# Optimization experiments

Hardware: AMD Instinct MI355X
Metric: run time of the kernel (lower is better)

## Reference

```python
import jax, jax.numpy as jnp
import numpy as np

HC = 64                 # half_context
PAD = HC + 3            # padding_idx row of positional table
NEG = 1.0e12            # additive mask constant from the torch code


def setup_inputs() -> dict:
    key = jax.random.key(0)
    ks = jax.random.split(key, 7)
    B, S, D, C = 32, 2048, 1024, 256
    embeds = jax.random.normal(ks[0], (B, S, D), dtype=jnp.float32)
    embeds_mask = jnp.ones((B, S), dtype=jnp.float32)
    latent = jax.random.normal(ks[1], (C, D), dtype=jnp.float32)
    att_diag = jax.random.normal(ks[2], (D,), dtype=jnp.float32)
    tok_diag = jax.random.normal(ks[3], (D,), dtype=jnp.float32)
    pos_table = jax.random.normal(ks[4], (2 * HC + 4, D), dtype=jnp.float32)
    pos_table = pos_table.at[PAD].set(0.0)  # padding_idx row is zeros
    tok_mult = jnp.ones((1,), dtype=jnp.float32)
    rel_pos_ids = jax.random.randint(ks[5], (B, S), 0, HC + 4, dtype=jnp.int32)
    return {
        "embeds": embeds,
        "embeds_mask": embeds_mask,
        "latent": latent,
        "att_diag": att_diag,
        "tok_diag": tok_diag,
        "pos_table": pos_table,
        "tok_mult": tok_mult,
        "rel_pos_ids": rel_pos_ids,
    }


def reference(embeds, embeds_mask, latent, att_diag, tok_diag, pos_table, tok_mult, rel_pos_ids):
    # positional-embedding gather and merge (dropouts are identity in eval)
    absolute_pos = rel_pos_ids + HC                       # [B,S]
    pos_embeds = pos_table[absolute_pos]                  # [B,S,D]
    merged = tok_mult[0] * embeds + pos_embeds            # [B,S,D]
    # entity-token attention scores: (latent * diag) @ merged^T
    scores = jnp.einsum('cd,bsd->bcs', latent * att_diag, merged)  # [B,C,S]
    m = embeds_mask[:, None, :]                           # [B,1,S]
    scores = scores * m + (m - 1.0) * NEG                 # mask-add
    top = jnp.max(scores, axis=1)                         # max over classes -> [B,S]
    att_probs = jax.nn.softmax(top, axis=1)               # softmax over tokens
    # weighted sum of (embeds * tok_diag) by attention probs -> [B,D]
    ctx_vecs = jnp.einsum('bsd,d,bs->bd', embeds, tok_diag, att_probs)
    return ctx_vecs
```

## Files before the change

### kernel.cpp

```cpp
#include <hip/hip_runtime.h>
#include <hip/hip_bf16.h>


#define HC 64
#define NEGV 1000000000000.0f

constexpr int Bb = 32, Ss = 2048, Dd = 1024, Cc = 256;
constexpr int NKC = 32;
constexpr int CT = Cc / 16;
constexpr int NBLK = 16;

typedef _Float16 f16x8 __attribute__((ext_vector_type(8)));
typedef float    f32x4 __attribute__((ext_vector_type(4)));

__global__ __launch_bounds__(256) void k_prep_w(
    const float* __restrict__ latent, const float* __restrict__ att_diag,
    _Float16* __restrict__ whi)
{
    const int idx = blockIdx.x * 256 + threadIdx.x;
    const int c = idx >> 10, k = idx & 1023;
    const float wv = latent[idx] * att_diag[k];
    const int kc = k >> 5, g = (k >> 3) & 3, i = k & 7;
    const int lane = (c & 15) + 16 * g, ct = c >> 4;
    whi[(size_t)kc * 8192 + (size_t)ct * 512 + lane * 8 + i] = (_Float16)wv;
}

__global__ __launch_bounds__(256, 2) void k_scores_mfma(
    const float* __restrict__ embeds,
    const float* __restrict__ mask,
    const float* __restrict__ pos_table,
    const float* __restrict__ tok_mult,
    const int*   __restrict__ rel_ids,
    const _Float16* __restrict__ whi,
    float* __restrict__ partial,
    float* __restrict__ mblk,
    float* __restrict__ zblk)
{
    __shared__ _Float16 sbuf[2][8192];
    __shared__ float l_sh[128];
    __shared__ float w_sh[128];
    __shared__ float red2[2];
    __shared__ float zred[2];

    const int t  = threadIdx.x;
    const int wv = t >> 6;
    const int l  = t & 63;
    const int lr = l & 15;
    const int lg = l >> 4;

    const int b   = blockIdx.x >> 4;
    const int blk = blockIdx.x & 15;
    const int s0  = blk * 128;

    const float tm = tok_mult[0];

    const float* erow[2];
    const float* prow[2];
    #pragma unroll
    for (int st = 0; st < 2; st++) {
        const int tok = s0 + wv * 32 + st * 16 + lr;
        erow[st] = embeds + ((size_t)b * Ss + tok) * Dd;
        prow[st] = pos_table + (size_t)(rel_ids[b * Ss + tok] + HC) * Dd;
    }

    f32x4 acc[CT][2];
    #pragma unroll
    for (int ct = 0; ct < CT; ct++)
        #pragma unroll
        for (int st = 0; st < 2; st++) acc[ct][st] = (f32x4){0.f, 0.f, 0.f, 0.f};

    f32x4 e0[2], e1[2], p0[2], p1[2];
    auto loadEP = [&](int kc) {
        const int k0 = kc * 32 + lg * 8;
        #pragma unroll
        for (int st = 0; st < 2; st++) {
            e0[st] = *(const f32x4*)(erow[st] + k0);
            e1[st] = *(const f32x4*)(erow[st] + k0 + 4);
            p0[st] = *(const f32x4*)(prow[st] + k0);
            p1[st] = *(const f32x4*)(prow[st] + k0 + 4);
        }
    };

    auto stage = [&](int kc, _Float16* dst) {
        const _Float16* src = whi + (size_t)kc * 8192;
        #pragma unroll
        for (int i = 0; i < 4; i++) {
            const int off = (i * 4 + wv) << 9;
            __builtin_amdgcn_global_load_lds(
                (const __attribute__((address_space(1))) void*)(src + off + l * 8),
                (__attribute__((address_space(3))) void*)(dst + off),
                16, 0, 0);
        }
    };

    stage(0, sbuf[0]);
    loadEP(0);
    asm volatile("s_waitcnt vmcnt(8)" ::: "memory");
    __builtin_amdgcn_s_barrier();

    int cur = 0;
    for (int kc = 0; kc < NKC; kc++) {
        if (kc + 1 < NKC) stage(kc + 1, sbuf[cur ^ 1]);

        f16x8 bh[2], bl[2];
        #pragma unroll
        for (int st = 0; st < 2; st++) {
            float e[8], p[8];
            *(f32x4*)&e[0] = e0[st]; *(f32x4*)&e[4] = e1[st];
            *(f32x4*)&p[0] = p0[st]; *(f32x4*)&p[4] = p1[st];
            #pragma unroll
            for (int i = 0; i < 8; i++) {
                const float x = fmaf(tm, e[i], p[i]);
                const _Float16 h = (_Float16)x;
                bh[st][i] = h;
                bl[st][i] = (_Float16)(x - (float)h);
            }
        }
        if (kc + 1 < NKC) loadEP(kc + 1);

        const _Float16* base = sbuf[cur];
        #pragma unroll
        for (int ct = 0; ct < CT; ct++) {
            const f16x8 ah = *(const f16x8*)(base + ct * 512 + l * 8);
            #pragma unroll
            for (int st = 0; st < 2; st++) {
                acc[ct][st] = __builtin_amdgcn_mfma_f32_16x16x32_f16(ah, bh[st], acc[ct][st], 0, 0, 0);
                acc[ct][st] = __builtin_amdgcn_mfma_f32_16x16x32_f16(ah, bl[st], acc[ct][st], 0, 0, 0);
            }
        }
        asm volatile("s_waitcnt vmcnt(8)" ::: "memory");
        __builtin_amdgcn_s_barrier();
        cur ^= 1;
    }

    #pragma unroll
    for (int st = 0; st < 2; st++) {
        float mx = acc[0][st][0];
        #pragma unroll
        for (int ct = 0; ct < CT; ct++)
            #pragma unroll
            for (int r = 0; r < 4; r++) mx = fmaxf(mx, acc[ct][st][r]);
        mx = fmaxf(mx, __shfl_xor(mx, 16));
        mx = fmaxf(mx, __shfl_xor(mx, 32));
        if (lg == 0) {
            const int si = wv * 32 + st * 16 + lr;
            const int s  = s0 + si;
            const float mk = mask[b * Ss + s];
            l_sh[si] = mx * mk + (mk - 1.0f) * NEGV;
        }
    }
    __syncthreads();

    if (t < 128) {
        float v = l_sh[t];
        #pragma unroll
        for (int o = 32; o >= 1; o >>= 1) v = fmaxf(v, __shfl_xor(v, o));
        if ((t & 63) == 0) red2[t >> 6] = v;
    }
    __syncthreads();
    const float Mb = fmaxf(red2[0], red2[1]);
    if (t < 128) w_sh[t] = expf(l_sh[t] - Mb);
    __syncthreads();
    if (t < 128) {
        float z = w_sh[t];
        #pragma unroll
        for (int o = 32; o >= 1; o >>= 1) z += __shfl_xor(z, o);
        if ((t & 63) == 0) zred[t >> 6] = z;
    }
    __syncthreads();

    {
        const float* eb = embeds + ((size_t)b * Ss + s0) * Dd + t * 4;
        f32x4 ca = (f32x4){0.f, 0.f, 0.f, 0.f};
        #pragma unroll 8
        for (int s = 0; s < 128; s++) {
            const float wgt = w_sh[s];
            const f32x4 ev = *(const f32x4*)(eb + (size_t)s * Dd);
            ca[0] = fmaf(wgt, ev[0], ca[0]);
            ca[1] = fmaf(wgt, ev[1], ca[1]);
            ca[2] = fmaf(wgt, ev[2], ca[2]);
            ca[3] = fmaf(wgt, ev[3], ca[3]);
        }
        *(f32x4*)(partial + ((size_t)(b * NBLK + blk)) * Dd + t * 4) = ca;
        if (t == 0) {
            mblk[b * NBLK + blk] = Mb;
            zblk[b * NBLK + blk] = zred[0] + zred[1];
        }
    }
}

__global__ __launch_bounds__(256) void k_finish(
    const float* __restrict__ mblk, const float* __restrict__ zblk,
    const float* __restrict__ partial, const float* __restrict__ tok_diag,
    float* __restrict__ out)
{
    __shared__ float cf[NBLK];
    const int b = blockIdx.x, t = threadIdx.x;

    if (t < 64) {
        const float mv = (t < NBLK) ? mblk[b * NBLK + t] : -3.4e38f;
        float M = mv;
        #pragma unroll
        for (int o = 32; o >= 1; o >>= 1) M = fmaxf(M, __shfl_xor(M, o));
        const float zv = (t < NBLK) ? zblk[b * NBLK + t] * expf(mv - M) : 0.f;
        float Z = zv;
        #pragma unroll
        for (int o = 32; o >= 1; o >>= 1) Z += __shfl_xor(Z, o);
        if (t < NBLK) cf[t] = expf(mv - M) / Z;
    }
    __syncthreads();

    const int d = t * 4;
    f32x4 a = (f32x4){0.f, 0.f, 0.f, 0.f};
    #pragma unroll
    for (int j = 0; j < NBLK; j++) {
        const float c = cf[j];
        const f32x4 p = *(const f32x4*)(partial + ((size_t)(b * NBLK + j)) * Dd + d);
        a[0] = fmaf(c, p[0], a[0]);
        a[1] = fmaf(c, p[1], a[1]);
        a[2] = fmaf(c, p[2], a[2]);
        a[3] = fmaf(c, p[3], a[3]);
    }
    const f32x4 td = *(const f32x4*)(tok_diag + d);
    f32x4 o = a * td;
    *(f32x4*)(out + (size_t)b * Dd + d) = o;
}

extern "C" void kernel_launch(void* const* d_in, const int* in_sizes, int n_in,
                              void* d_out, int out_size, void* d_ws, size_t ws_size,
                              hipStream_t stream) {
    const float* embeds    = (const float*)d_in[0];
    const float* mask      = (const float*)d_in[1];
    const float* latent    = (const float*)d_in[2];
    const float* att_diag  = (const float*)d_in[3];
    const float* tok_diag  = (const float*)d_in[4];
    const float* pos_table = (const float*)d_in[5];
    const float* tok_mult  = (const float*)d_in[6];
    const int*   rel_ids   = (const int*)d_in[7];
    float* out = (float*)d_out;

    char* ws = (char*)d_ws;
    _Float16* whi    = (_Float16*)(ws);
    float*    partial= (float*)(ws + 524288);
    float*    mblk   = (float*)(ws + 2621440);
    float*    zblk   = (float*)(ws + 2623488);

    k_prep_w<<<(Cc * Dd) / 256, 256, 0, stream>>>(latent, att_diag, whi);
    k_scores_mfma<<<Bb * NBLK, 256, 0, stream>>>(
        embeds, mask, pos_table, tok_mult, rel_ids, whi, partial, mblk, zblk);
    k_finish<<<Bb, 256, 0, stream>>>(mblk, zblk, partial, tok_diag, out);
}
```

Measured before the change: 121.9 us.

## Split class tiles across two waves per token group with 512-thread blocks

Doubles the block to 512 threads and splits the 256 classes between wave pairs, so each wave holds half the accumulators (8 tiles instead of 16). Per-wave register use drops, which allows launch bounds of 4 blocks per CU and more waves to hide memory latency. Positional rows are now loaded inside the loop instead of prefetched, and each token sub-tile is converted and multiplied in turn. The cost is that embeds and positional rows are loaded twice, once per class half, and an extra shared-memory max merge is needed.

After: 194.6 us. +59.6%, slower.

```diff
diff --git a/kernel.cpp b/kernel.cpp
--- a/kernel.cpp
+++ b/kernel.cpp
@@ -7,11 +7,11 @@
 
 constexpr int Bb = 32, Ss = 2048, Dd = 1024, Cc = 256;
 constexpr int NKC = 32;
-constexpr int CT = Cc / 16;
 constexpr int NBLK = 16;
 
 typedef _Float16 f16x8 __attribute__((ext_vector_type(8)));
 typedef float    f32x4 __attribute__((ext_vector_type(4)));
+typedef float    f32x2 __attribute__((ext_vector_type(2)));
 
 __global__ __launch_bounds__(256) void k_prep_w(
     const float* __restrict__ latent, const float* __restrict__ att_diag,
@@ -25,7 +25,7 @@
     whi[(size_t)kc * 8192 + (size_t)ct * 512 + lane * 8 + i] = (_Float16)wv;
 }
 
-__global__ __launch_bounds__(256, 2) void k_scores_mfma(
+__global__ __launch_bounds__(512, 4) void k_scores_mfma(
     const float* __restrict__ embeds,
     const float* __restrict__ mask,
     const float* __restrict__ pos_table,
@@ -37,13 +37,14 @@
     float* __restrict__ zblk)
 {
     __shared__ _Float16 sbuf[2][8192];
-    __shared__ float l_sh[128];
+    __shared__ float red[2][128];
     __shared__ float w_sh[128];
-    __shared__ float red2[2];
-    __shared__ float zred[2];
+    __shared__ float red2[2], zred[2];
 
     const int t  = threadIdx.x;
-    const int wv = t >> 6;
+    const int wvid = t >> 6;
+    const int cg = wvid & 1;
+    const int tg = wvid >> 1;
     const int l  = t & 63;
     const int lr = l & 15;
     const int lg = l >> 4;
@@ -58,34 +59,32 @@
     const float* prow[2];
     #pragma unroll
     for (int st = 0; st < 2; st++) {
-        const int tok = s0 + wv * 32 + st * 16 + lr;
+        const int tok = s0 + tg * 32 + st * 16 + lr;
         erow[st] = embeds + ((size_t)b * Ss + tok) * Dd;
         prow[st] = pos_table + (size_t)(rel_ids[b * Ss + tok] + HC) * Dd;
     }
 
-    f32x4 acc[CT][2];
-    #pragma unroll
-    for (int ct = 0; ct < CT; ct++)
-        #pragma unroll
-        for (int st = 0; st < 2; st++) acc[ct][st] = (f32x4){0.f, 0.f, 0.f, 0.f};
-
-    f32x4 e0[2], e1[2], p0[2], p1[2];
-    auto loadEP = [&](int kc) {
+    f32x4 acc[8][2];
+    #pragma unroll
+    for (int j = 0; j < 8; j++)
+        #pragma unroll
+        for (int st = 0; st < 2; st++) acc[j][st] = (f32x4){0.f, 0.f, 0.f, 0.f};
+
+    f32x4 e0[2], e1[2];
+    auto loadE = [&](int kc) {
         const int k0 = kc * 32 + lg * 8;
         #pragma unroll
         for (int st = 0; st < 2; st++) {
             e0[st] = *(const f32x4*)(erow[st] + k0);
             e1[st] = *(const f32x4*)(erow[st] + k0 + 4);
-            p0[st] = *(const f32x4*)(prow[st] + k0);
-            p1[st] = *(const f32x4*)(prow[st] + k0 + 4);
         }
     };
 
     auto stage = [&](int kc, _Float16* dst) {
         const _Float16* src = whi + (size_t)kc * 8192;
         #pragma unroll
-        for (int i = 0; i < 4; i++) {
-            const int off = (i * 4 + wv) << 9;
+        for (int i = 0; i < 2; i++) {
+            const int off = (i * 8 + wvid) << 9;
             __builtin_amdgcn_global_load_lds(
                 (const __attribute__((address_space(1))) void*)(src + off + l * 8),
                 (__attribute__((address_space(3))) void*)(dst + off),
@@ -94,41 +93,60 @@
     };
 
     stage(0, sbuf[0]);
-    loadEP(0);
-    asm volatile("s_waitcnt vmcnt(8)" ::: "memory");
+    loadE(0);
+    asm volatile("s_waitcnt vmcnt(4)" ::: "memory");
     __builtin_amdgcn_s_barrier();
 
     int cur = 0;
     for (int kc = 0; kc < NKC; kc++) {
-        if (kc + 1 < NKC) stage(kc + 1, sbuf[cur ^ 1]);
-
-        f16x8 bh[2], bl[2];
-        #pragma unroll
-        for (int st = 0; st < 2; st++) {
+        const int k0 = kc * 32 + lg * 8;
+        const _Float16* base = sbuf[cur] + (cg * 8) * 512 + l * 8;
+
+        {
+            const f32x4 pa = *(const f32x4*)(prow[0] + k0);
+            const f32x4 pb = *(const f32x4*)(prow[0] + k0 + 4);
             float e[8], p[8];
-            *(f32x4*)&e[0] = e0[st]; *(f32x4*)&e[4] = e1[st];
-            *(f32x4*)&p[0] = p0[st]; *(f32x4*)&p[4] = p1[st];
+            *(f32x4*)&e[0] = e0[0]; *(f32x4*)&e[4] = e1[0];
+            *(f32x4*)&p[0] = pa;    *(f32x4*)&p[4] = pb;
+            f16x8 bh, bl;
             #pragma unroll
             for (int i = 0; i < 8; i++) {
                 const float x = fmaf(tm, e[i], p[i]);
                 const _Float16 h = (_Float16)x;
-                bh[st][i] = h;
-                bl[st][i] = (_Float16)(x - (float)h);
-            }
-        }
-        if (kc + 1 < NKC) loadEP(kc + 1);
-
-        const _Float16* base = sbuf[cur];
-        #pragma unroll
-        for (int ct = 0; ct < CT; ct++) {
-            const f16x8 ah = *(const f16x8*)(base + ct * 512 + l * 8);
-            #pragma unroll
-            for (int st = 0; st < 2; st++) {
-                acc[ct][st] = __builtin_amdgcn_mfma_f32_16x16x32_f16(ah, bh[st], acc[ct][st], 0, 0, 0);
-                acc[ct][st] = __builtin_amdgcn_mfma_f32_16x16x32_f16(ah, bl[st], acc[ct][st], 0, 0, 0);
-            }
-        }
-        asm volatile("s_waitcnt vmcnt(8)" ::: "memory");
+                bh[i] = h;
+                bl[i] = (_Float16)(x - (float)h);
+            }
+            if (kc + 1 < NKC) stage(kc + 1, sbuf[cur ^ 1]);
+            #pragma unroll
+            for (int j = 0; j < 8; j++) {
+                const f16x8 ah = *(const f16x8*)(base + j * 512);
+                acc[j][0] = __builtin_amdgcn_mfma_f32_16x16x32_f16(ah, bh, acc[j][0], 0, 0, 0);
+                acc[j][0] = __builtin_amdgcn_mfma_f32_16x16x32_f16(ah, bl, acc[j][0], 0, 0, 0);
+            }
+        }
+        {
+            const f32x4 pa = *(const f32x4*)(prow[1] + k0);
+            const f32x4 pb = *(const f32x4*)(prow[1] + k0 + 4);
+            float e[8], p[8];
+            *(f32x4*)&e[0] = e0[1]; *(f32x4*)&e[4] = e1[1];
+            *(f32x4*)&p[0] = pa;    *(f32x4*)&p[4] = pb;
+            f16x8 bh, bl;
+            #pragma unroll
+            for (int i = 0; i < 8; i++) {
+                const float x = fmaf(tm, e[i], p[i]);
+                const _Float16 h = (_Float16)x;
+                bh[i] = h;
+                bl[i] = (_Float16)(x - (float)h);
+            }
+            if (kc + 1 < NKC) loadE(kc + 1);
+            #pragma unroll
+            for (int j = 0; j < 8; j++) {
+                const f16x8 ah = *(const f16x8*)(base + j * 512);
+                acc[j][1] = __builtin_amdgcn_mfma_f32_16x16x32_f16(ah, bh, acc[j][1], 0, 0, 0);
+                acc[j][1] = __builtin_amdgcn_mfma_f32_16x16x32_f16(ah, bl, acc[j][1], 0, 0, 0);
+            }
+        }
+        asm volatile("s_waitcnt vmcnt(4)" ::: "memory");
         __builtin_amdgcn_s_barrier();
         cur ^= 1;
     }
@@ -137,29 +155,28 @@
     for (int st = 0; st < 2; st++) {
         float mx = acc[0][st][0];
         #pragma unroll
-        for (int ct = 0; ct < CT; ct++)
-            #pragma unroll
-            for (int r = 0; r < 4; r++) mx = fmaxf(mx, acc[ct][st][r]);
+        for (int j = 0; j < 8; j++)
+            #pragma unroll
+            for (int r = 0; r < 4; r++) mx = fmaxf(mx, acc[j][st][r]);
         mx = fmaxf(mx, __shfl_xor(mx, 16));
         mx = fmaxf(mx, __shfl_xor(mx, 32));
-        if (lg == 0) {
-            const int si = wv * 32 + st * 16 + lr;
-            const int s  = s0 + si;
-            const float mk = mask[b * Ss + s];
-            l_sh[si] = mx * mk + (mk - 1.0f) * NEGV;
-        }
+        if (lg == 0) red[cg][tg * 32 + st * 16 + lr] = mx;
     }
     __syncthreads();
 
     if (t < 128) {
-        float v = l_sh[t];
+        const int s = s0 + t;
+        const float mk = mask[b * Ss + s];
+        const float lv = fmaxf(red[0][t], red[1][t]) * mk + (mk - 1.0f) * NEGV;
+        red[0][t] = lv;
+        float v = lv;
         #pragma unroll
         for (int o = 32; o >= 1; o >>= 1) v = fmaxf(v, __shfl_xor(v, o));
         if ((t & 63) == 0) red2[t >> 6] = v;
     }
     __syncthreads();
     const float Mb = fmaxf(red2[0], red2[1]);
-    if (t < 128) w_sh[t] = expf(l_sh[t] - Mb);
+    if (t < 128) w_sh[t] = expf(red[0][t] - Mb);
     __syncthreads();
     if (t < 128) {
         float z = w_sh[t];
@@ -170,18 +187,16 @@
     __syncthreads();
 
     {
-        const float* eb = embeds + ((size_t)b * Ss + s0) * Dd + t * 4;
-        f32x4 ca = (f32x4){0.f, 0.f, 0.f, 0.f};
+        const float* eb = embeds + ((size_t)b * Ss + s0) * Dd + t * 2;
+        f32x2 ca = (f32x2){0.f, 0.f};
         #pragma unroll 8
         for (int s = 0; s < 128; s++) {
             const float wgt = w_sh[s];
-            const f32x4 ev = *(const f32x4*)(eb + (size_t)s * Dd);
+            const f32x2 ev = *(const f32x2*)(eb + (size_t)s * Dd);
             ca[0] = fmaf(wgt, ev[0], ca[0]);
             ca[1] = fmaf(wgt, ev[1], ca[1]);
-            ca[2] = fmaf(wgt, ev[2], ca[2]);
-            ca[3] = fmaf(wgt, ev[3], ca[3]);
-        }
-        *(f32x4*)(partial + ((size_t)(b * NBLK + blk)) * Dd + t * 4) = ca;
+        }
+        *(f32x2*)(partial + ((size_t)(b * NBLK + blk)) * Dd + t * 2) = ca;
         if (t == 0) {
             mblk[b * NBLK + blk] = Mb;
             zblk[b * NBLK + blk] = zred[0] + zred[1];
@@ -246,7 +261,7 @@
     float*    zblk   = (float*)(ws + 2623488);
 
     k_prep_w<<<(Cc * Dd) / 256, 256, 0, stream>>>(latent, att_diag, whi);
-    k_scores_mfma<<<Bb * NBLK, 256, 0, stream>>>(
+    k_scores_mfma<<<Bb * NBLK, 512, 0, stream>>>(
         embeds, mask, pos_table, tok_mult, rel_ids, whi, partial, mblk, zblk);
     k_finish<<<Bb, 256, 0, stream>>>(mblk, zblk, partial, tok_diag, out);
 }
```

## Double K-chunk size and split MFMA loop into barrier-separated quarters with setprio

Applied to the files above, without the earlier changes.

The main loop now processes 64 K-elements per iteration, staging twice as much of the weight tile into LDS (32 KB per buffer) and holding two sets of embed/pos register prefetches. Each iteration is split into four MFMA quarters separated by workgroup barriers, with s_setprio raised around MFMA bursts and global loads interleaved between quarters. The aim is to halve loop overhead and synchronization count per K and to overlap global loads with MFMA more finely. In exchange it raises LDS use to 64 KB and register pressure from the doubled prefetch buffers, which may reduce occupancy under launch_bounds(256,2).

Result: no change. 123.0 us (+0.9%).

```diff
diff --git a/kernel.cpp b/kernel.cpp
--- a/kernel.cpp
+++ b/kernel.cpp
@@ -8,6 +8,7 @@
 constexpr int Bb = 32, Ss = 2048, Dd = 1024, Cc = 256;
 constexpr int NKC = 32;
 constexpr int CT = Cc / 16;
+constexpr int NOUT = 16;
 constexpr int NBLK = 16;
 
 typedef _Float16 f16x8 __attribute__((ext_vector_type(8)));
@@ -36,11 +37,10 @@
     float* __restrict__ mblk,
     float* __restrict__ zblk)
 {
-    __shared__ _Float16 sbuf[2][8192];
+    __shared__ _Float16 sbuf[2][16384];
     __shared__ float l_sh[128];
     __shared__ float w_sh[128];
-    __shared__ float red2[2];
-    __shared__ float zred[2];
+    __shared__ float red2[2], zred[2];
 
     const int t  = threadIdx.x;
     const int wv = t >> 6;
@@ -69,22 +69,33 @@
         #pragma unroll
         for (int st = 0; st < 2; st++) acc[ct][st] = (f32x4){0.f, 0.f, 0.f, 0.f};
 
-    f32x4 e0[2], e1[2], p0[2], p1[2];
-    auto loadEP = [&](int kc) {
-        const int k0 = kc * 32 + lg * 8;
+    f32x4 eA0[2], eA1[2], pA0[2], pA1[2];
+    f32x4 eB0[2], eB1[2], pB0[2], pB1[2];
+    auto loadEP_A = [&](int out) {
+        const int k0 = out * 64 + lg * 8;
         #pragma unroll
         for (int st = 0; st < 2; st++) {
-            e0[st] = *(const f32x4*)(erow[st] + k0);
-            e1[st] = *(const f32x4*)(erow[st] + k0 + 4);
-            p0[st] = *(const f32x4*)(prow[st] + k0);
-            p1[st] = *(const f32x4*)(prow[st] + k0 + 4);
-        }
-    };
-
-    auto stage = [&](int kc, _Float16* dst) {
-        const _Float16* src = whi + (size_t)kc * 8192;
-        #pragma unroll
-        for (int i = 0; i < 4; i++) {
+            eA0[st] = *(const f32x4*)(erow[st] + k0);
+            eA1[st] = *(const f32x4*)(erow[st] + k0 + 4);
+            pA0[st] = *(const f32x4*)(prow[st] + k0);
+            pA1[st] = *(const f32x4*)(prow[st] + k0 + 4);
+        }
+    };
+    auto loadEP_B = [&](int out) {
+        const int k0 = out * 64 + 32 + lg * 8;
+        #pragma unroll
+        for (int st = 0; st < 2; st++) {
+            eB0[st] = *(const f32x4*)(erow[st] + k0);
+            eB1[st] = *(const f32x4*)(erow[st] + k0 + 4);
+            pB0[st] = *(const f32x4*)(prow[st] + k0);
+            pB1[st] = *(const f32x4*)(prow[st] + k0 + 4);
+        }
+    };
+
+    auto stage = [&](int out, _Float16* dst) {
+        const _Float16* src = whi + (size_t)out * 16384;
+        #pragma unroll
+        for (int i = 0; i < 8; i++) {
             const int off = (i * 4 + wv) << 9;
             __builtin_amdgcn_global_load_lds(
                 (const __attribute__((address_space(1))) void*)(src + off + l * 8),
@@ -93,21 +104,13 @@
         }
     };
 
-    stage(0, sbuf[0]);
-    loadEP(0);
-    asm volatile("s_waitcnt vmcnt(8)" ::: "memory");
-    __builtin_amdgcn_s_barrier();
-
-    int cur = 0;
-    for (int kc = 0; kc < NKC; kc++) {
-        if (kc + 1 < NKC) stage(kc + 1, sbuf[cur ^ 1]);
-
-        f16x8 bh[2], bl[2];
+    auto build = [&](const f32x4* E0, const f32x4* E1, const f32x4* P0,
+                     const f32x4* P1, f16x8* bh, f16x8* bl) {
         #pragma unroll
         for (int st = 0; st < 2; st++) {
             float e[8], p[8];
-            *(f32x4*)&e[0] = e0[st]; *(f32x4*)&e[4] = e1[st];
-            *(f32x4*)&p[0] = p0[st]; *(f32x4*)&p[4] = p1[st];
+            *(f32x4*)&e[0] = E0[st]; *(f32x4*)&e[4] = E1[st];
+            *(f32x4*)&p[0] = P0[st]; *(f32x4*)&p[4] = P1[st];
             #pragma unroll
             for (int i = 0; i < 8; i++) {
                 const float x = fmaf(tm, e[i], p[i]);
@@ -116,19 +119,58 @@
                 bl[st][i] = (_Float16)(x - (float)h);
             }
         }
-        if (kc + 1 < NKC) loadEP(kc + 1);
-
-        const _Float16* base = sbuf[cur];
-        #pragma unroll
-        for (int ct = 0; ct < CT; ct++) {
-            const f16x8 ah = *(const f16x8*)(base + ct * 512 + l * 8);
-            #pragma unroll
-            for (int st = 0; st < 2; st++) {
-                acc[ct][st] = __builtin_amdgcn_mfma_f32_16x16x32_f16(ah, bh[st], acc[ct][st], 0, 0, 0);
-                acc[ct][st] = __builtin_amdgcn_mfma_f32_16x16x32_f16(ah, bl[st], acc[ct][st], 0, 0, 0);
+    };
+
+    auto quarter = [&](const _Float16* base, int ct0, const f16x8* bh, const f16x8* bl) {
+        #pragma unroll
+        for (int g4 = 0; g4 < 2; g4++) {
+            f16x8 ah[4];
+            #pragma unroll
+            for (int j = 0; j < 4; j++)
+                ah[j] = *(const f16x8*)(base + (ct0 + g4 * 4 + j) * 512 + l * 8);
+            __builtin_amdgcn_s_setprio(1);
+            #pragma unroll
+            for (int j = 0; j < 4; j++) {
+                const int ct = ct0 + g4 * 4 + j;
+                #pragma unroll
+                for (int st = 0; st < 2; st++) {
+                    acc[ct][st] = __builtin_amdgcn_mfma_f32_16x16x32_f16(ah[j], bh[st], acc[ct][st], 0, 0, 0);
+                    acc[ct][st] = __builtin_amdgcn_mfma_f32_16x16x32_f16(ah[j], bl[st], acc[ct][st], 0, 0, 0);
+                }
             }
-        }
-        asm volatile("s_waitcnt vmcnt(8)" ::: "memory");
+            __builtin_amdgcn_s_setprio(0);
+        }
+    };
+
+    stage(0, sbuf[0]);
+    loadEP_A(0);
+    loadEP_B(0);
+    asm volatile("s_waitcnt vmcnt(16)" ::: "memory");
+    __builtin_amdgcn_s_barrier();
+
+    int cur = 0;
+    for (int out = 0; out < NOUT; out++) {
+        const bool more = (out + 1 < NOUT);
+        const _Float16* base0 = sbuf[cur];
+        const _Float16* base1 = sbuf[cur] + 8192;
+        f16x8 bh0[2], bl0[2], bh1[2], bl1[2];
+
+        if (more) stage(out + 1, sbuf[cur ^ 1]);
+        build(eA0, eA1, pA0, pA1, bh0, bl0);
+        quarter(base0, 0, bh0, bl0);
+        __builtin_amdgcn_s_barrier();
+
+        if (more) loadEP_A(out + 1);
+        quarter(base0, 8, bh0, bl0);
+        __builtin_amdgcn_s_barrier();
+
+        build(eB0, eB1, pB0, pB1, bh1, bl1);
+        if (more) loadEP_B(out + 1);
+        quarter(base1, 0, bh1, bl1);
+        __builtin_amdgcn_s_barrier();
+
+        quarter(base1, 8, bh1, bl1);
+        asm volatile("s_waitcnt vmcnt(16)" ::: "memory");
         __builtin_amdgcn_s_barrier();
         cur ^= 1;
     }
```

## Precompute positional score table to drop per-token pos_table gathers

Applied to the files above, without the earlier changes.

Uses linearity of the score matmul: W·(tm·e + p) = (tm·W)·e + W·p. A new small kernel precomputes W·p for all 132 positional rows into a [132,256] table, and tok_mult is folded into the fp16 weights. The main kernel then loads only embeds in its K loop and adds the gathered table row before the class max. This removes half of the per-token global loads and the fused multiply-add in the hot loop, at the cost of an extra launch and a slightly different rounding path, since tm is now rounded into fp16 weights.

Result: slower. 154.3 us (+26.6%).

```diff
diff --git a/kernel.cpp b/kernel.cpp
--- a/kernel.cpp
+++ b/kernel.cpp
@@ -15,23 +15,56 @@
 
 __global__ __launch_bounds__(256) void k_prep_w(
     const float* __restrict__ latent, const float* __restrict__ att_diag,
-    _Float16* __restrict__ whi)
+    const float* __restrict__ tok_mult, _Float16* __restrict__ whi)
 {
     const int idx = blockIdx.x * 256 + threadIdx.x;
     const int c = idx >> 10, k = idx & 1023;
-    const float wv = latent[idx] * att_diag[k];
+    const float wv = tok_mult[0] * latent[idx] * att_diag[k];
     const int kc = k >> 5, g = (k >> 3) & 3, i = k & 7;
     const int lane = (c & 15) + 16 * g, ct = c >> 4;
     whi[(size_t)kc * 8192 + (size_t)ct * 512 + lane * 8 + i] = (_Float16)wv;
 }
 
+__global__ __launch_bounds__(256) void k_wp(
+    const float* __restrict__ latent, const float* __restrict__ att_diag,
+    const float* __restrict__ pos_table, float* __restrict__ wpt)
+{
+    __shared__ float pa[1024];
+    const int pid = blockIdx.x;
+    const int t = threadIdx.x;
+    {
+        f32x4 p4 = *(const f32x4*)(pos_table + (size_t)pid * Dd + t * 4);
+        f32x4 a4 = *(const f32x4*)(att_diag + t * 4);
+        *(f32x4*)&pa[t * 4] = p4 * a4;
+    }
+    __syncthreads();
+    const int wv = t >> 6, l = t & 63;
+    float pav[16];
+    #pragma unroll
+    for (int q = 0; q < 4; q++) *(f32x4*)&pav[q * 4] = *(const f32x4*)&pa[l * 16 + q * 4];
+    for (int c = wv; c < Cc; c += 4) {
+        const float* lrow = latent + (size_t)c * Dd + l * 16;
+        float s = 0.f;
+        #pragma unroll
+        for (int q = 0; q < 4; q++) {
+            f32x4 lv = *(const f32x4*)(lrow + q * 4);
+            s = fmaf(lv[0], pav[q * 4 + 0], s);
+            s = fmaf(lv[1], pav[q * 4 + 1], s);
+            s = fmaf(lv[2], pav[q * 4 + 2], s);
+            s = fmaf(lv[3], pav[q * 4 + 3], s);
+        }
+        #pragma unroll
+        for (int o = 32; o >= 1; o >>= 1) s += __shfl_xor(s, o);
+        if (l == 0) wpt[pid * Cc + c] = s;
+    }
+}
+
 __global__ __launch_bounds__(256, 2) void k_scores_mfma(
     const float* __restrict__ embeds,
     const float* __restrict__ mask,
-    const float* __restrict__ pos_table,
-    const float* __restrict__ tok_mult,
     const int*   __restrict__ rel_ids,
     const _Float16* __restrict__ whi,
+    const float* __restrict__ wpt,
     float* __restrict__ partial,
     float* __restrict__ mblk,
     float* __restrict__ zblk)
@@ -39,8 +72,7 @@
     __shared__ _Float16 sbuf[2][8192];
     __shared__ float l_sh[128];
     __shared__ float w_sh[128];
-    __shared__ float red2[2];
-    __shared__ float zred[2];
+    __shared__ float red2[2], zred[2];
 
     const int t  = threadIdx.x;
     const int wv = t >> 6;
@@ -52,15 +84,13 @@
     const int blk = blockIdx.x & 15;
     const int s0  = blk * 128;
 
-    const float tm = tok_mult[0];
-
     const float* erow[2];
-    const float* prow[2];
+    int pid[2];
     #pragma unroll
     for (int st = 0; st < 2; st++) {
         const int tok = s0 + wv * 32 + st * 16 + lr;
         erow[st] = embeds + ((size_t)b * Ss + tok) * Dd;
-        prow[st] = pos_table + (size_t)(rel_ids[b * Ss + tok] + HC) * Dd;
+        pid[st]  = rel_ids[b * Ss + tok] + HC;
     }
 
     f32x4 acc[CT][2];
@@ -69,15 +99,13 @@
         #pragma unroll
         for (int st = 0; st < 2; st++) acc[ct][st] = (f32x4){0.f, 0.f, 0.f, 0.f};
 
-    f32x4 e0[2], e1[2], p0[2], p1[2];
-    auto loadEP = [&](int kc) {
+    f32x4 e0[2], e1[2];
+    auto loadE = [&](int kc) {
         const int k0 = kc * 32 + lg * 8;
         #pragma unroll
         for (int st = 0; st < 2; st++) {
             e0[st] = *(const f32x4*)(erow[st] + k0);
             e1[st] = *(const f32x4*)(erow[st] + k0 + 4);
-            p0[st] = *(const f32x4*)(prow[st] + k0);
-            p1[st] = *(const f32x4*)(prow[st] + k0 + 4);
         }
     };
 
@@ -94,8 +122,8 @@
     };
 
     stage(0, sbuf[0]);
-    loadEP(0);
-    asm volatile("s_waitcnt vmcnt(8)" ::: "memory");
+    loadE(0);
+    asm volatile("s_waitcnt vmcnt(4)" ::: "memory");
     __builtin_amdgcn_s_barrier();
 
     int cur = 0;
@@ -105,18 +133,16 @@
         f16x8 bh[2], bl[2];
         #pragma unroll
         for (int st = 0; st < 2; st++) {
-            float e[8], p[8];
+            float e[8];
             *(f32x4*)&e[0] = e0[st]; *(f32x4*)&e[4] = e1[st];
-            *(f32x4*)&p[0] = p0[st]; *(f32x4*)&p[4] = p1[st];
             #pragma unroll
             for (int i = 0; i < 8; i++) {
-                const float x = fmaf(tm, e[i], p[i]);
-                const _Float16 h = (_Float16)x;
+                const _Float16 h = (_Float16)e[i];
                 bh[st][i] = h;
-                bl[st][i] = (_Float16)(x - (float)h);
+                bl[st][i] = (_Float16)(e[i] - (float)h);
             }
         }
-        if (kc + 1 < NKC) loadEP(kc + 1);
+        if (kc + 1 < NKC) loadE(kc + 1);
 
         const _Float16* base = sbuf[cur];
         #pragma unroll
@@ -128,18 +154,21 @@
                 acc[ct][st] = __builtin_amdgcn_mfma_f32_16x16x32_f16(ah, bl[st], acc[ct][st], 0, 0, 0);
             }
         }
-        asm volatile("s_waitcnt vmcnt(8)" ::: "memory");
+        asm volatile("s_waitcnt vmcnt(4)" ::: "memory");
         __builtin_amdgcn_s_barrier();
         cur ^= 1;
     }
 
     #pragma unroll
     for (int st = 0; st < 2; st++) {
-        float mx = acc[0][st][0];
-        #pragma unroll
-        for (int ct = 0; ct < CT; ct++)
+        const float* wrow = wpt + pid[st] * Cc + lg * 4;
+        float mx = -3.4e38f;
+        #pragma unroll
+        for (int ct = 0; ct < CT; ct++) {
+            const f32x4 wp = *(const f32x4*)(wrow + ct * 16);
             #pragma unroll
-            for (int r = 0; r < 4; r++) mx = fmaxf(mx, acc[ct][st][r]);
+            for (int r = 0; r < 4; r++) mx = fmaxf(mx, acc[ct][st][r] + wp[r]);
+        }
         mx = fmaxf(mx, __shfl_xor(mx, 16));
         mx = fmaxf(mx, __shfl_xor(mx, 32));
         if (lg == 0) {
@@ -241,12 +270,14 @@
 
     char* ws = (char*)d_ws;
     _Float16* whi    = (_Float16*)(ws);
-    float*    partial= (float*)(ws + 524288);
-    float*    mblk   = (float*)(ws + 2621440);
-    float*    zblk   = (float*)(ws + 2623488);
-
-    k_prep_w<<<(Cc * Dd) / 256, 256, 0, stream>>>(latent, att_diag, whi);
+    float*    wpt    = (float*)(ws + 524288);
+    float*    partial= (float*)(ws + 786432);
+    float*    mblk   = (float*)(ws + 2883584);
+    float*    zblk   = (float*)(ws + 2885632);
+
+    k_prep_w<<<(Cc * Dd) / 256, 256, 0, stream>>>(latent, att_diag, tok_mult, whi);
+    k_wp<<<132, 256, 0, stream>>>(latent, att_diag, pos_table, wpt);
     k_scores_mfma<<<Bb * NBLK, 256, 0, stream>>>(
-        embeds, mask, pos_table, tok_mult, rel_ids, whi, partial, mblk, zblk);
+        embeds, mask, rel_ids, whi, wpt, partial, mblk, zblk);
     k_finish<<<Bb, 256, 0, stream>>>(mblk, zblk, partial, tok_diag, out);
 }
```
